# Performance work log

Measured on AMD Instinct MI355X. Metric: run time of the kernel, lower is better.

Reference implementation:

```python
import jax, jax.numpy as jnp
import numpy as np

E = 8        # num_expert
D = 768      # d_model
H = 3072     # expert hidden = 4*d_model
K = 2        # top_k
N = 4096     # tokens
C = 2048


def setup_inputs() -> dict:
    key = jax.random.key(0)
    k0, k1, k2, k3 = jax.random.split(key, 4)
    moe_inp = jax.random.normal(k0, (N, D), dtype=jnp.float32)
    gate_w = jax.random.normal(k1, (D, E), dtype=jnp.float32) / np.sqrt(D).astype(np.float32)
    gate_b = jnp.zeros((E,), dtype=jnp.float32)
    w1 = jax.random.normal(k2, (E, D, H), dtype=jnp.float32) / np.sqrt(D).astype(np.float32)
    b1 = jnp.zeros((E, H), dtype=jnp.float32)
    w2 = jax.random.normal(k3, (E, H, D), dtype=jnp.float32) / np.sqrt(H).astype(np.float32)
    b2 = jnp.zeros((E, D), dtype=jnp.float32)
    return {"moe_inp": moe_inp, "gate_w": gate_w, "gate_b": gate_b,
            "w1": w1, "b1": b1, "w2": w2, "b2": b2}


def reference(moe_inp, gate_w, gate_b, w1, b1, w2, b2):
    # --- NaiveGate: linear scores, top-k experts, softmax over the k scores ---
    logits = moe_inp @ gate_w + gate_b                      # [N, E]
    top_v, top_i = jax.lax.top_k(logits, K)                 # [N, K]
    gate_score = jax.nn.softmax(top_v, axis=-1)             # [N, K]

    # --- scatter tokens to expert-contiguous capacity buffers (MOEScatter) ---
    flat_e = top_i.reshape(-1)                              # [N*K] expert id per slot
    onehot = jax.nn.one_hot(flat_e, E, dtype=jnp.int32)     # [N*K, E]
    # running position of each token inside its expert's buffer
    pos = jnp.sum(jnp.cumsum(onehot, axis=0) * onehot, axis=1) - 1  # [N*K]
    x_rep = jnp.repeat(moe_inp, K, axis=0)                  # [N*K, D]
    xe = jnp.zeros((E, C, D), dtype=moe_inp.dtype).at[flat_e, pos].set(x_rep, mode='drop')

    # --- grouped expert FFN (expert_fn): per-expert batched GEMMs ---
    h = jax.nn.gelu(jnp.einsum('ecd,edh->ech', xe, w1) + b1[:, None, :])
    ye = jnp.einsum('ech,ehd->ecd', h, w2) + b2[:, None, :]  # [E, C, D]

    # --- gather back to token order (MOEGather) and combine with gate scores ---
    y_flat = ye.at[flat_e, pos].get(mode='fill', fill_value=0.0)  # [N*K, D]
    out = jnp.einsum('nkd,nk->nd', y_flat.reshape(N, K, D), gate_score)
    return out
```

## Files before the change

kernel.cpp:

```cpp
#include <hip/hip_runtime.h>
#include <hip/hip_bf16.h>
#include <math.h>

#define NT    4096
#define DM    768
#define HD    3072
#define NE    8
#define CAP   2048
#define SLOTS_MAX 9216

typedef __attribute__((ext_vector_type(8))) short bf16x8;
typedef __attribute__((ext_vector_type(4))) float f32x4;

__device__ __forceinline__ unsigned short f2bf(float f) {
  unsigned int u = __float_as_uint(f);
  unsigned int r = (u + 0x7fffu + ((u >> 16) & 1u)) >> 16;
  return (unsigned short)r;
}

__device__ __forceinline__ void async16(const unsigned short* g, unsigned short* l) {
  __builtin_amdgcn_global_load_lds((const __attribute__((address_space(1))) void*)g,
                                   (__attribute__((address_space(3))) void*)l,
                                   16, 0, 0);
}

__global__ void convert_x_kernel(const float* __restrict__ x,
                                 unsigned short* __restrict__ xb) {
  int i = (blockIdx.x * 256 + threadIdx.x) * 4;
  float4 v = *(const float4*)(x + i);
  uint2 o;
  o.x = (unsigned int)f2bf(v.x) | ((unsigned int)f2bf(v.y) << 16);
  o.y = (unsigned int)f2bf(v.z) | ((unsigned int)f2bf(v.w) << 16);
  *(uint2*)(xb + i) = o;
}

__global__ void transpose_kernel(const float* __restrict__ src,
                                 unsigned short* __restrict__ dst,
                                 int R, int src_stride, int col_off,
                                 size_t src_e_stride, size_t dst_e_stride) {
  __shared__ unsigned short tile[64][34];
  const float* s = src + blockIdx.z * src_e_stride;
  unsigned short* d = dst + blockIdx.z * dst_e_stride;
  const int r0 = blockIdx.y * 32;
  const int c0 = blockIdx.x * 64;
  const int t = threadIdx.x;
#pragma unroll
  for (int i = 0; i < 4; i++) {
    int row = (t >> 5) + i * 8;
    int cu  = t & 31;
    const float2 v = *(const float2*)(s + (size_t)(r0 + row) * src_stride + col_off + c0 + cu * 2);
    tile[cu * 2][row]     = f2bf(v.x);
    tile[cu * 2 + 1][row] = f2bf(v.y);
  }
  __syncthreads();
#pragma unroll
  for (int i = 0; i < 4; i++) {
    int drow = (t >> 4) + i * 16;
    int ru   = t & 15;
    unsigned int v = *(const unsigned int*)&tile[drow][ru * 2];
    *(unsigned int*)(d + (size_t)(c0 + drow) * R + r0 + ru * 2) = v;
  }
}

__global__ void gate_dots_kernel(const float* __restrict__ inp,
                                 const float* __restrict__ gw,
                                 const float* __restrict__ gb,
                                 int2* __restrict__ tope,
                                 float2* __restrict__ tops) {
  const int tok  = blockIdx.x * 4 + (threadIdx.x >> 6);
  const int lane = threadIdx.x & 63;
  const float* x = inp + (size_t)tok * DM;
  float acc[NE];
#pragma unroll
  for (int e = 0; e < NE; e++) acc[e] = 0.f;
  for (int d = lane; d < DM; d += 64) {
    float xv = x[d];
    const float4 w0 = *(const float4*)(gw + d * NE);
    const float4 w1v = *(const float4*)(gw + d * NE + 4);
    acc[0] += xv * w0.x; acc[1] += xv * w0.y;
    acc[2] += xv * w0.z; acc[3] += xv * w0.w;
    acc[4] += xv * w1v.x; acc[5] += xv * w1v.y;
    acc[6] += xv * w1v.z; acc[7] += xv * w1v.w;
  }
#pragma unroll
  for (int e = 0; e < NE; e++) {
    float v = acc[e];
#pragma unroll
    for (int m = 32; m > 0; m >>= 1) v += __shfl_xor(v, m, 64);
    acc[e] = v + gb[e];
  }
  if (lane == 0) {
    float bv = -1e30f, sv = -1e30f; int bi = 0, si = 0;
#pragma unroll
    for (int e = 0; e < NE; e++) {
      float v = acc[e];
      if (v > bv)      { sv = bv; si = bi; bv = v; bi = e; }
      else if (v > sv) { sv = v;  si = e; }
    }
    float e1 = expf(sv - bv);
    float s0 = 1.f / (1.f + e1);
    float s1 = e1 / (1.f + e1);
    tope[tok] = make_int2(bi, si);
    tops[tok] = make_float2(s0, s1);
  }
}

__global__ void assign_kernel(const int2* __restrict__ tope,
                              const float2* __restrict__ tops,
                              int* __restrict__ cnt,
                              int* __restrict__ base,
                              int* __restrict__ src,
                              float* __restrict__ scale) {
  __shared__ int lcnt[NE];
  const int t = threadIdx.x;
  if (t < NE) lcnt[t] = 0;
  __syncthreads();
  for (int i = t; i < NT; i += 1024) {
    int2 e = tope[i];
    float2 s = tops[i];
    int p0 = atomicAdd(&lcnt[e.x], 1);
    if (p0 < CAP) { src[e.x * CAP + p0] = i; scale[e.x * CAP + p0] = s.x; }
    int p1 = atomicAdd(&lcnt[e.y], 1);
    if (p1 < CAP) { src[e.y * CAP + p1] = i; scale[e.y * CAP + p1] = s.y; }
  }
  __syncthreads();
  if (t == 0) {
    int b = 0;
    for (int e = 0; e < NE; e++) {
      int c = min(lcnt[e], CAP);
      cnt[e] = c;
      base[e] = b;
      b += (c + 127) & ~127;
    }
  }
}

__global__ __launch_bounds__(256) void gemm1_kernel(
    const unsigned short* __restrict__ xb,
    const unsigned short* __restrict__ w1t,
    const float* __restrict__ b1,
    const int* __restrict__ cnt,
    const int* __restrict__ base,
    const int* __restrict__ src,
    unsigned short* __restrict__ h,
    int hoff, int chunk) {
  const int e = blockIdx.z;
  const int count = cnt[e];
  const int m0 = blockIdx.y * 128;
  if (m0 >= count) return;
  const int n0 = blockIdx.x * 128;
  const int hb = base[e];

  __shared__ unsigned short As[128 * 32];
  __shared__ unsigned short Bs[128 * 32];

  const int t = threadIdx.x;
  const int lane = t & 63;
  const int wave = t >> 6;
  const int r0 = t >> 2;
  const int kc = (t & 3) * 8;

  const int tok0 = src[e * CAP + m0 + r0];
  const int tok1 = src[e * CAP + m0 + r0 + 64];
  const unsigned short* aptr0 = xb + (size_t)tok0 * DM + kc;
  const unsigned short* aptr1 = xb + (size_t)tok1 * DM + kc;
  const unsigned short* w1e = w1t + (size_t)e * chunk * DM;
  const unsigned short* bptr0 = w1e + (size_t)(n0 + r0) * DM + kc;
  const unsigned short* bptr1 = bptr0 + (size_t)64 * DM;

  unsigned short* as0 = As + (wave * 64) * 8;
  unsigned short* as1 = As + (256 + wave * 64) * 8;
  unsigned short* bs0 = Bs + (wave * 64) * 8;
  unsigned short* bs1 = Bs + (256 + wave * 64) * 8;

  const int wrow = (wave >> 1) * 64;
  const int wcol = (wave & 1) * 64;
  const int lrow = lane & 15;
  const int koff = (lane >> 4) * 8;

  f32x4 acc[4][4];
#pragma unroll
  for (int i = 0; i < 4; i++)
#pragma unroll
    for (int j = 0; j < 4; j++) acc[i][j] = (f32x4){0.f, 0.f, 0.f, 0.f};

  for (int k0 = 0; k0 < DM; k0 += 32) {
    async16(aptr0 + k0, as0);
    async16(aptr1 + k0, as1);
    async16(bptr0 + k0, bs0);
    async16(bptr1 + k0, bs1);
    __syncthreads();
    bf16x8 af[4], bfr[4];
#pragma unroll
    for (int i = 0; i < 4; i++)
      af[i] = *(const bf16x8*)(As + (wrow + i * 16 + lrow) * 32 + koff);
#pragma unroll
    for (int j = 0; j < 4; j++)
      bfr[j] = *(const bf16x8*)(Bs + (wcol + j * 16 + lrow) * 32 + koff);
#pragma unroll
    for (int i = 0; i < 4; i++)
#pragma unroll
      for (int j = 0; j < 4; j++)
        acc[i][j] = __builtin_amdgcn_mfma_f32_16x16x32_bf16(af[i], bfr[j], acc[i][j], 0, 0, 0);
    __syncthreads();
  }

  const int q4 = (lane >> 4) * 4;
  const int c = lane & 15;
  unsigned short* hrow = h + (size_t)(hb + m0) * chunk + n0;
#pragma unroll
  for (int j = 0; j < 4; j++) {
    const float bias = b1[e * HD + hoff + n0 + wcol + j * 16 + c];
#pragma unroll
    for (int i = 0; i < 4; i++) {
#pragma unroll
      for (int r = 0; r < 4; r++) {
        int m = wrow + i * 16 + q4 + r;
        float v = acc[i][j][r] + bias;
        float g = 0.5f * v * (1.f + tanhf(0.7978845608f * (v + 0.044715f * v * v * v)));
        hrow[(size_t)m * chunk + wcol + j * 16 + c] = f2bf(g);
      }
    }
  }
}

__global__ __launch_bounds__(256) void gemm2_kernel(
    const unsigned short* __restrict__ h,
    const unsigned short* __restrict__ w2t,
    const float* __restrict__ b2,
    const int* __restrict__ cnt,
    const int* __restrict__ base,
    const int* __restrict__ src,
    const float* __restrict__ scale,
    float* __restrict__ out,
    int chunk, int add_b2) {
  const int e = blockIdx.z;
  const int count = cnt[e];
  const int m0 = blockIdx.y * 128;
  if (m0 >= count) return;
  const int n0 = blockIdx.x * 128;
  const int hb = base[e];

  __shared__ unsigned short As[128 * 32];
  __shared__ unsigned short Bs[128 * 32];

  const int t = threadIdx.x;
  const int lane = t & 63;
  const int wave = t >> 6;
  const int r0 = t >> 2;
  const int kc = (t & 3) * 8;

  const unsigned short* aptr0 = h + (size_t)(hb + m0 + r0) * chunk + kc;
  const unsigned short* aptr1 = aptr0 + (size_t)64 * chunk;
  const unsigned short* w2e = w2t + (size_t)e * DM * chunk;
  const unsigned short* bptr0 = w2e + (size_t)(n0 + r0) * chunk + kc;
  const unsigned short* bptr1 = bptr0 + (size_t)64 * chunk;

  unsigned short* as0 = As + (wave * 64) * 8;
  unsigned short* as1 = As + (256 + wave * 64) * 8;
  unsigned short* bs0 = Bs + (wave * 64) * 8;
  unsigned short* bs1 = Bs + (256 + wave * 64) * 8;

  const int wrow = (wave >> 1) * 64;
  const int wcol = (wave & 1) * 64;
  const int lrow = lane & 15;
  const int koff = (lane >> 4) * 8;

  f32x4 acc[4][4];
#pragma unroll
  for (int i = 0; i < 4; i++)
#pragma unroll
    for (int j = 0; j < 4; j++) acc[i][j] = (f32x4){0.f, 0.f, 0.f, 0.f};

  for (int k0 = 0; k0 < chunk; k0 += 32) {
    async16(aptr0 + k0, as0);
    async16(aptr1 + k0, as1);
    async16(bptr0 + k0, bs0);
    async16(bptr1 + k0, bs1);
    __syncthreads();
    bf16x8 af[4], bfr[4];
#pragma unroll
    for (int i = 0; i < 4; i++)
      af[i] = *(const bf16x8*)(As + (wrow + i * 16 + lrow) * 32 + koff);
#pragma unroll
    for (int j = 0; j < 4; j++)
      bfr[j] = *(const bf16x8*)(Bs + (wcol + j * 16 + lrow) * 32 + koff);
#pragma unroll
    for (int i = 0; i < 4; i++)
#pragma unroll
      for (int j = 0; j < 4; j++)
        acc[i][j] = __builtin_amdgcn_mfma_f32_16x16x32_bf16(af[i], bfr[j], acc[i][j], 0, 0, 0);
    __syncthreads();
  }

  const int q4 = (lane >> 4) * 4;
  const int c = lane & 15;
#pragma unroll
  for (int i = 0; i < 4; i++) {
#pragma unroll
    for (int r = 0; r < 4; r++) {
      int m = m0 + wrow + i * 16 + q4 + r;
      float sc = scale[e * CAP + m];
      int tok = src[e * CAP + m];
      float* orow = out + (size_t)tok * DM + n0;
#pragma unroll
      for (int j = 0; j < 4; j++) {
        int n = wcol + j * 16 + c;
        float v = acc[i][j][r];
        if (add_b2) v += b2[e * DM + n0 + n];
        atomicAdd(&orow[n], sc * v);
      }
    }
  }
}

extern "C" void kernel_launch(void* const* d_in, const int* in_sizes, int n_in,
                              void* d_out, int out_size, void* d_ws, size_t ws_size,
                              hipStream_t stream) {
  const float* inp = (const float*)d_in[0];
  const float* gw  = (const float*)d_in[1];
  const float* gb  = (const float*)d_in[2];
  const float* w1  = (const float*)d_in[3];
  const float* b1  = (const float*)d_in[4];
  const float* w2  = (const float*)d_in[5];
  const float* b2  = (const float*)d_in[6];
  float* out = (float*)d_out;

  const int cands[8] = {3072, 1536, 1024, 768, 512, 384, 256, 128};
  int chunk = 128;
  const size_t meta = 197120;
  for (int ci = 0; ci < 8; ci++) {
    int c = cands[ci];
    size_t need = meta + (size_t)NT * DM * 2 + 2 * (size_t)NE * c * DM * 2
                + (size_t)SLOTS_MAX * c * 2;
    if (need <= ws_size) { chunk = c; break; }
  }

  char* ws = (char*)d_ws;
  int*    cnt  = (int*)(ws);
  int*    base = (int*)(ws + 256);
  int*    srcb = (int*)(ws + 512);
  float*  scl  = (float*)(ws + 66048);
  int2*   tope = (int2*)(ws + 131584);
  float2* tops = (float2*)(ws + 164352);
  size_t off = meta;
  unsigned short* xb = (unsigned short*)(ws + off);   off += (size_t)NT * DM * 2;
  unsigned short* w1tc = (unsigned short*)(ws + off); off += (size_t)NE * chunk * DM * 2;
  unsigned short* w2tc = (unsigned short*)(ws + off); off += (size_t)NE * chunk * DM * 2;
  unsigned short* hc = (unsigned short*)(ws + off);

  hipMemsetAsync(ws, 0, 131584, stream);
  hipMemsetAsync(out, 0, (size_t)NT * DM * 4, stream);

  convert_x_kernel<<<(NT * DM) / 1024, 256, 0, stream>>>(inp, xb);
  gate_dots_kernel<<<NT / 4, 256, 0, stream>>>(inp, gw, gb, tope, tops);
  assign_kernel<<<1, 1024, 0, stream>>>(tope, tops, cnt, base, srcb, scl);

  for (int c = 0; c < HD; c += chunk) {
    transpose_kernel<<<dim3(chunk / 64, DM / 32, NE), 256, 0, stream>>>(
        w1, w1tc, DM, HD, c, (size_t)DM * HD, (size_t)chunk * DM);
    transpose_kernel<<<dim3(DM / 64, chunk / 32, NE), 256, 0, stream>>>(
        w2 + (size_t)c * DM, w2tc, chunk, DM, 0, (size_t)HD * DM, (size_t)DM * chunk);
    gemm1_kernel<<<dim3(chunk / 128, CAP / 128, NE), 256, 0, stream>>>(
        xb, w1tc, b1, cnt, base, srcb, hc, c, chunk);
    gemm2_kernel<<<dim3(DM / 128, CAP / 128, NE), 256, 0, stream>>>(
        hc, w2tc, b2, cnt, base, srcb, scl, out, chunk, c == 0 ? 1 : 0);
  }
}
```

Before: 448.3 us.

## Replace atomic scatter-add with expert-buffer output plus gather kernel, interleave experts in grid

GEMM2 now writes per-expert results into a dense fp32 ye buffer instead of doing float atomicAdds into the token-ordered output. A new gather kernel then combines the two expert rows per token with their gate scores, and the output memset is dropped. The assign kernel uses wave-aggregated shared atomics and records per-token positions. The GEMM grids are flattened so the expert index varies fastest. GELU switches to the equivalent sigmoid/__expf form, and out-of-range rows are guarded. The extra fp32 ye buffer adds memory traffic and a read-modify-write per chunk when chunk is smaller than HD.

```diff
diff --git a/kernel.cpp b/kernel.cpp
--- a/kernel.cpp
+++ b/kernel.cpp
@@ -105,23 +105,40 @@
   }
 }
 
+__device__ __forceinline__ int agg_inc(int* lcnt, int key) {
+  const int lane = threadIdx.x & 63;
+  int p = 0;
+#pragma unroll
+  for (int ee = 0; ee < NE; ee++) {
+    unsigned long long m = __ballot(key == ee);
+    if (m) {
+      int leader = __ffsll(m) - 1;
+      int n = __popcll(m);
+      int b = 0;
+      if (lane == leader) b = atomicAdd(&lcnt[ee], n);
+      b = __shfl(b, leader, 64);
+      if (key == ee) p = b + __popcll(m & ((1ull << lane) - 1ull));
+    }
+  }
+  return p;
+}
+
 __global__ void assign_kernel(const int2* __restrict__ tope,
-                              const float2* __restrict__ tops,
                               int* __restrict__ cnt,
                               int* __restrict__ base,
                               int* __restrict__ src,
-                              float* __restrict__ scale) {
+                              int2* __restrict__ pos) {
   __shared__ int lcnt[NE];
   const int t = threadIdx.x;
   if (t < NE) lcnt[t] = 0;
   __syncthreads();
   for (int i = t; i < NT; i += 1024) {
     int2 e = tope[i];
-    float2 s = tops[i];
-    int p0 = atomicAdd(&lcnt[e.x], 1);
-    if (p0 < CAP) { src[e.x * CAP + p0] = i; scale[e.x * CAP + p0] = s.x; }
-    int p1 = atomicAdd(&lcnt[e.y], 1);
-    if (p1 < CAP) { src[e.y * CAP + p1] = i; scale[e.y * CAP + p1] = s.y; }
+    int p0 = agg_inc(lcnt, e.x);
+    int p1 = agg_inc(lcnt, e.y);
+    if (p0 < CAP) src[e.x * CAP + p0] = i;
+    if (p1 < CAP) src[e.y * CAP + p1] = i;
+    pos[i] = make_int2(p0, p1);
   }
   __syncthreads();
   if (t == 0) {
@@ -144,11 +161,13 @@
     const int* __restrict__ src,
     unsigned short* __restrict__ h,
     int hoff, int chunk) {
-  const int e = blockIdx.z;
+  const int b = blockIdx.x;
+  const int e = b & 7;
+  const int idx = b >> 3;
+  const int m0 = (idx & 15) * 128;
+  const int n0 = (idx >> 4) * 128;
   const int count = cnt[e];
-  const int m0 = blockIdx.y * 128;
   if (m0 >= count) return;
-  const int n0 = blockIdx.x * 128;
   const int hb = base[e];
 
   __shared__ unsigned short As[128 * 32];
@@ -160,8 +179,8 @@
   const int r0 = t >> 2;
   const int kc = (t & 3) * 8;
 
-  const int tok0 = src[e * CAP + m0 + r0];
-  const int tok1 = src[e * CAP + m0 + r0 + 64];
+  const int tok0 = (m0 + r0      < count) ? src[e * CAP + m0 + r0]      : 0;
+  const int tok1 = (m0 + r0 + 64 < count) ? src[e * CAP + m0 + r0 + 64] : 0;
   const unsigned short* aptr0 = xb + (size_t)tok0 * DM + kc;
   const unsigned short* aptr1 = xb + (size_t)tok1 * DM + kc;
   const unsigned short* w1e = w1t + (size_t)e * chunk * DM;
@@ -217,7 +236,8 @@
       for (int r = 0; r < 4; r++) {
         int m = wrow + i * 16 + q4 + r;
         float v = acc[i][j][r] + bias;
-        float g = 0.5f * v * (1.f + tanhf(0.7978845608f * (v + 0.044715f * v * v * v)));
+        float u2 = 1.5957691216f * (v + 0.044715f * v * v * v);
+        float g = v / (1.f + __expf(-u2));
         hrow[(size_t)m * chunk + wcol + j * 16 + c] = f2bf(g);
       }
     }
@@ -230,15 +250,15 @@
     const float* __restrict__ b2,
     const int* __restrict__ cnt,
     const int* __restrict__ base,
-    const int* __restrict__ src,
-    const float* __restrict__ scale,
-    float* __restrict__ out,
+    float* __restrict__ ye,
     int chunk, int add_b2) {
-  const int e = blockIdx.z;
+  const int b = blockIdx.x;
+  const int e = b & 7;
+  const int idx = b >> 3;
+  const int m0 = (idx & 15) * 128;
+  const int n0 = (idx >> 4) * 128;
   const int count = cnt[e];
-  const int m0 = blockIdx.y * 128;
   if (m0 >= count) return;
-  const int n0 = blockIdx.x * 128;
   const int hb = base[e];
 
   __shared__ unsigned short As[128 * 32];
@@ -295,23 +315,45 @@
 
   const int q4 = (lane >> 4) * 4;
   const int c = lane & 15;
+  float* yrow = ye + (size_t)(hb + m0) * DM + n0;
 #pragma unroll
   for (int i = 0; i < 4; i++) {
 #pragma unroll
     for (int r = 0; r < 4; r++) {
-      int m = m0 + wrow + i * 16 + q4 + r;
-      float sc = scale[e * CAP + m];
-      int tok = src[e * CAP + m];
-      float* orow = out + (size_t)tok * DM + n0;
+      int m = wrow + i * 16 + q4 + r;
 #pragma unroll
       for (int j = 0; j < 4; j++) {
         int n = wcol + j * 16 + c;
         float v = acc[i][j][r];
-        if (add_b2) v += b2[e * DM + n0 + n];
-        atomicAdd(&orow[n], sc * v);
+        v += add_b2 ? b2[e * DM + n0 + n] : yrow[(size_t)m * DM + n];
+        yrow[(size_t)m * DM + n] = v;
       }
     }
   }
+}
+
+__global__ void gather_kernel(const float* __restrict__ ye,
+                              const int2* __restrict__ tope,
+                              const float2* __restrict__ tops,
+                              const int2* __restrict__ pos,
+                              const int* __restrict__ base,
+                              float* __restrict__ out) {
+  int idx = blockIdx.x * 256 + threadIdx.x;
+  int tok = idx / (DM / 4);
+  int d4 = (idx % (DM / 4)) * 4;
+  int2 e = tope[tok];
+  float2 s = tops[tok];
+  int2 p = pos[tok];
+  float4 r = make_float4(0.f, 0.f, 0.f, 0.f);
+  if (p.x < CAP) {
+    const float4 v = *(const float4*)(ye + (size_t)(base[e.x] + p.x) * DM + d4);
+    r.x += s.x * v.x; r.y += s.x * v.y; r.z += s.x * v.z; r.w += s.x * v.w;
+  }
+  if (p.y < CAP) {
+    const float4 v = *(const float4*)(ye + (size_t)(base[e.y] + p.y) * DM + d4);
+    r.x += s.y * v.x; r.y += s.y * v.y; r.z += s.y * v.z; r.w += s.y * v.w;
+  }
+  *(float4*)(out + (size_t)tok * DM + d4) = r;
 }
 
 extern "C" void kernel_launch(void* const* d_in, const int* in_sizes, int n_in,
@@ -326,13 +368,15 @@
   const float* b2  = (const float*)d_in[6];
   float* out = (float*)d_out;
 
+  const size_t meta = 164352;
   const int cands[8] = {3072, 1536, 1024, 768, 512, 384, 256, 128};
   int chunk = 128;
-  const size_t meta = 197120;
   for (int ci = 0; ci < 8; ci++) {
     int c = cands[ci];
-    size_t need = meta + (size_t)NT * DM * 2 + 2 * (size_t)NE * c * DM * 2
-                + (size_t)SLOTS_MAX * c * 2;
+    size_t need = meta + (size_t)NT * DM * 2
+                + 2 * (size_t)NE * c * DM * 2
+                + (size_t)SLOTS_MAX * c * 2
+                + (size_t)SLOTS_MAX * DM * 4;
     if (need <= ws_size) { chunk = c; break; }
   }
 
@@ -340,30 +384,30 @@
   int*    cnt  = (int*)(ws);
   int*    base = (int*)(ws + 256);
   int*    srcb = (int*)(ws + 512);
-  float*  scl  = (float*)(ws + 66048);
-  int2*   tope = (int2*)(ws + 131584);
-  float2* tops = (float2*)(ws + 164352);
+  int2*   tope = (int2*)(ws + 66048);
+  float2* tops = (float2*)(ws + 98816);
+  int2*   pos  = (int2*)(ws + 131584);
   size_t off = meta;
   unsigned short* xb = (unsigned short*)(ws + off);   off += (size_t)NT * DM * 2;
   unsigned short* w1tc = (unsigned short*)(ws + off); off += (size_t)NE * chunk * DM * 2;
   unsigned short* w2tc = (unsigned short*)(ws + off); off += (size_t)NE * chunk * DM * 2;
-  unsigned short* hc = (unsigned short*)(ws + off);
-
-  hipMemsetAsync(ws, 0, 131584, stream);
-  hipMemsetAsync(out, 0, (size_t)NT * DM * 4, stream);
+  unsigned short* hc = (unsigned short*)(ws + off);   off += (size_t)SLOTS_MAX * chunk * 2;
+  float* ye = (float*)(ws + off);
 
   convert_x_kernel<<<(NT * DM) / 1024, 256, 0, stream>>>(inp, xb);
   gate_dots_kernel<<<NT / 4, 256, 0, stream>>>(inp, gw, gb, tope, tops);
-  assign_kernel<<<1, 1024, 0, stream>>>(tope, tops, cnt, base, srcb, scl);
+  assign_kernel<<<1, 1024, 0, stream>>>(tope, cnt, base, srcb, pos);
 
   for (int c = 0; c < HD; c += chunk) {
     transpose_kernel<<<dim3(chunk / 64, DM / 32, NE), 256, 0, stream>>>(
         w1, w1tc, DM, HD, c, (size_t)DM * HD, (size_t)chunk * DM);
     transpose_kernel<<<dim3(DM / 64, chunk / 32, NE), 256, 0, stream>>>(
         w2 + (size_t)c * DM, w2tc, chunk, DM, 0, (size_t)HD * DM, (size_t)DM * chunk);
-    gemm1_kernel<<<dim3(chunk / 128, CAP / 128, NE), 256, 0, stream>>>(
+    gemm1_kernel<<<NE * 16 * (chunk / 128), 256, 0, stream>>>(
         xb, w1tc, b1, cnt, base, srcb, hc, c, chunk);
-    gemm2_kernel<<<dim3(DM / 128, CAP / 128, NE), 256, 0, stream>>>(
-        hc, w2tc, b2, cnt, base, srcb, scl, out, chunk, c == 0 ? 1 : 0);
-  }
-}
+    gemm2_kernel<<<NE * 16 * (DM / 128), 256, 0, stream>>>(
+        hc, w2tc, b2, cnt, base, ye, chunk, c == 0 ? 1 : 0);
+  }
+
+  gather_kernel<<<(NT * DM / 4) / 256, 256, 0, stream>>>(ye, tope, tops, pos, base, out);
+}
```

Measured after the change: 397.3 us. -11.4%, faster.
